# Kernel optimization log

Hardware: AMD Instinct MI355X
Metric: run time of the kernel (lower is better)

Reference implementation:

```python
import jax, jax.numpy as jnp
import numpy as np

HIDDEN = 2048
N_HEADS = 16
HEAD_DIM = HIDDEN // N_HEADS
ROPE_THETA = 10000.0
BSZ, SEQ = 2, 2048
NEG_INF = -1e9


def setup_inputs() -> dict:
    key = jax.random.key(0)
    ks = jax.random.split(key, 5)
    scale = 1.0 / np.sqrt(HIDDEN)
    hidden_states = jax.random.normal(ks[0], (BSZ, SEQ, HIDDEN), dtype=jnp.float32)
    Wq = jax.random.normal(ks[1], (HIDDEN, HIDDEN), dtype=jnp.float32) * scale
    Wk = jax.random.normal(ks[2], (HIDDEN, HIDDEN), dtype=jnp.float32) * scale
    Wv = jax.random.normal(ks[3], (HIDDEN, HIDDEN), dtype=jnp.float32) * scale
    Wo = jax.random.normal(ks[4], (HIDDEN, HIDDEN), dtype=jnp.float32) * scale
    # additive causal mask, [1, 1, S, S]
    causal = jnp.triu(jnp.full((SEQ, SEQ), NEG_INF, dtype=jnp.float32), k=1)
    attention_mask = causal[None, None, :, :]
    position_ids = jnp.arange(SEQ, dtype=jnp.int32)
    return {
        "hidden_states": hidden_states,
        "Wq": Wq, "Wk": Wk, "Wv": Wv, "Wo": Wo,
        "attention_mask": attention_mask,
        "position_ids": position_ids,
    }


def _rotate_half(x):
    half = x.shape[-1] // 2
    return jnp.concatenate((-x[..., half:], x[..., :half]), axis=-1)


def _rope_tables(seq_len, position_ids):
    # inv_freq: [head_dim/2]
    inv_freq = 1.0 / (ROPE_THETA ** (jnp.arange(0, HEAD_DIM, 2, dtype=jnp.float32) / HEAD_DIM))
    t = jnp.arange(seq_len, dtype=jnp.float32)
    freqs = t[:, None] * inv_freq[None, :]              # [S, D/2]
    emb = jnp.concatenate((freqs, freqs), axis=-1)      # [S, D]
    cos = jnp.cos(emb)[position_ids]                    # [S, D]
    sin = jnp.sin(emb)[position_ids]
    return cos, sin


def reference(hidden_states, Wq, Wk, Wv, Wo, attention_mask, position_ids):
    b, s, h = hidden_states.shape
    def proj(W):
        return (hidden_states @ W.T).reshape(b, s, N_HEADS, HEAD_DIM).transpose(0, 2, 1, 3)
    q = proj(Wq)  # [B, H, S, D]
    k = proj(Wk)
    v = proj(Wv)
    cos, sin = _rope_tables(s, position_ids)            # [S, D], broadcasts over B,H
    q = q * cos + _rotate_half(q) * sin
    k = k * cos + _rotate_half(k) * sin
    scores = jnp.einsum('bhqd,bhkd->bhqk', q, k) / np.sqrt(HEAD_DIM)
    scores = scores + attention_mask
    w = jax.nn.softmax(scores, axis=-1)
    out = jnp.einsum('bhqk,bhkd->bhqd', w, v)           # [B, H, S, D]
    out = out.transpose(0, 2, 1, 3).reshape(b, s, h)
    return out @ Wo.T
```

## Files before the change

kernel.cpp:

```cpp
#include <hip/hip_runtime.h>
#include <cstdint>
#include <cstddef>

typedef __bf16 bf16;
typedef __bf16 bf16x4 __attribute__((ext_vector_type(4)));
typedef __bf16 bf16x8 __attribute__((ext_vector_type(8)));
typedef float  f32x4  __attribute__((ext_vector_type(4)));
typedef short  s16x4  __attribute__((ext_vector_type(4)));

#define HIDDEN 2048
#define NHEADS 16
#define HDIM   128
#define BSZ    2
#define SEQ    2048
#define BS     (BSZ*SEQ)
#define QKW    (2*HIDDEN)

union b4u { bf16x4 h; s16x4 s; };

__device__ __forceinline__ void async16(const bf16* g, bf16* l) {
    __builtin_amdgcn_global_load_lds(
        (const __attribute__((address_space(1))) unsigned int*)g,
        (__attribute__((address_space(3))) unsigned int*)l, 16, 0, 0);
}

__global__ __launch_bounds__(256) void cast_all(const float* __restrict__ hs,
                                                const float* __restrict__ Wq,
                                                const float* __restrict__ Wk,
                                                const float* __restrict__ Wv,
                                                const float* __restrict__ Wo,
                                                const int* __restrict__ pos,
                                                bf16* __restrict__ hs_b,
                                                bf16* __restrict__ wqkv,
                                                bf16* __restrict__ wo_b,
                                                float2* __restrict__ tab) {
    int i = blockIdx.x * 256 + threadIdx.x;
    if (i >= 6291456) {
        int j = i - 6291456;
        int s = j >> 6, p = j & 63;
        float t = (float)pos[s];
        float inv = expf(-(float)(2 * p) * (9.2103403719761836f / 128.0f));
        float sn, cs;
        sincosf(t * inv, &sn, &cs);
        tab[j] = make_float2(cs, sn);
        return;
    }
    const float* src; bf16* dst; int off;
    if (i < 2097152) { src = hs; dst = hs_b; off = i; }
    else {
        int j = i - 2097152;
        int r = j >> 20;
        off = j & 1048575;
        if      (r == 0) { src = Wq; dst = wqkv; }
        else if (r == 1) { src = Wk; dst = wqkv + (size_t)4194304; }
        else if (r == 2) { src = Wv; dst = wqkv + (size_t)8388608; }
        else             { src = Wo; dst = wo_b; }
    }
    const float4 v = ((const float4*)src)[off];
    bf16x4 o;
    o.x = (bf16)v.x; o.y = (bf16)v.y; o.z = (bf16)v.z; o.w = (bf16)v.w;
    ((bf16x4*)dst)[off] = o;
}

__global__ __launch_bounds__(256) void gemm_qkv(const bf16* __restrict__ A,
                                                const bf16* __restrict__ Bt,
                                                const float2* __restrict__ tab,
                                                bf16* __restrict__ qk,
                                                bf16* __restrict__ vtb) {
    __shared__ bf16 Als[128 * 32];
    __shared__ bf16 Bls[128 * 32];
    const int K    = HIDDEN;
    const int tid  = threadIdx.x;
    const int lane = tid & 63;
    const int w    = tid >> 6;
    const int l15  = lane & 15;
    const int quad = lane >> 4;
    const int mTile = blockIdx.y * 128;
    const int nTile = blockIdx.x * 128;
    const int wm = (w >> 1) * 64;
    const int wv = w & 1;

    f32x4 acc[4][4];
#pragma unroll
    for (int i = 0; i < 4; ++i)
#pragma unroll
        for (int j = 0; j < 4; ++j) acc[i][j] = (f32x4){0.f, 0.f, 0.f, 0.f};

    const bf16* gA = A + (size_t)(mTile + w * 32 + (lane >> 2)) * K + (lane & 3) * 8;
    const bf16* gB = Bt + (size_t)(nTile + w * 32 + (lane >> 2)) * K + (lane & 3) * 8;
    bf16* lA = Als + w * 1024;
    bf16* lB = Bls + w * 1024;

    for (int k0 = 0; k0 < K; k0 += 32) {
        async16(gA + k0,          lA);
        async16(gA + 16 * K + k0, lA + 512);
        async16(gB + k0,          lB);
        async16(gB + 16 * K + k0, lB + 512);
        __syncthreads();

        bf16x8 af[4], bfr[4];
#pragma unroll
        for (int mi = 0; mi < 4; ++mi)
            af[mi] = *(const bf16x8*)(Als + (wm + mi * 16 + l15) * 32 + quad * 8);
#pragma unroll
        for (int ni = 0; ni < 4; ++ni) {
            int co = wv * 32 + (ni & 1) * 16 + (ni >> 1) * 64;
            bfr[ni] = *(const bf16x8*)(Bls + (co + l15) * 32 + quad * 8);
        }
#pragma unroll
        for (int mi = 0; mi < 4; ++mi)
#pragma unroll
            for (int ni = 0; ni < 4; ++ni)
                acc[mi][ni] = __builtin_amdgcn_mfma_f32_16x16x32_bf16(
                    af[mi], bfr[ni], acc[mi][ni], 0, 0, 0);
        __syncthreads();
    }

    if (nTile < QKW) {
#pragma unroll
        for (int mi = 0; mi < 4; ++mi)
#pragma unroll
            for (int r = 0; r < 4; ++r) {
                int row = mTile + wm + mi * 16 + quad * 4 + r;
                int s   = row & (SEQ - 1);
                float2 t0 = tab[s * 64 + wv * 32 + l15];
                float2 t1 = tab[s * 64 + wv * 32 + 16 + l15];
                size_t rb = (size_t)row * QKW + nTile + wv * 32 + l15;
                float lo0 = acc[mi][0][r], hi0 = acc[mi][2][r];
                float lo1 = acc[mi][1][r], hi1 = acc[mi][3][r];
                qk[rb]      = (bf16)(lo0 * t0.x - hi0 * t0.y);
                qk[rb + 64] = (bf16)(hi0 * t0.x + lo0 * t0.y);
                qk[rb + 16] = (bf16)(lo1 * t1.x - hi1 * t1.y);
                qk[rb + 80] = (bf16)(hi1 * t1.x + lo1 * t1.y);
            }
    } else {
#pragma unroll
        for (int mi = 0; mi < 4; ++mi)
#pragma unroll
            for (int ni = 0; ni < 4; ++ni) {
                int col_v = (nTile - QKW) + wv * 32 + (ni & 1) * 16 + (ni >> 1) * 64 + l15;
                int row0  = mTile + wm + mi * 16 + quad * 4;
                bf16x4 pk;
#pragma unroll
                for (int r = 0; r < 4; ++r) pk[r] = (bf16)acc[mi][ni][r];
                *(bf16x4*)(vtb + (size_t)col_v * BS + row0) = pk;
            }
    }
}

template <typename OutT>
__global__ __launch_bounds__(256) void gemm_bt(const bf16* __restrict__ A,
                                               const bf16* __restrict__ Bt,
                                               OutT* __restrict__ C,
                                               int M, int N, int K) {
    __shared__ bf16 Als[128 * 32];
    __shared__ bf16 Bls[128 * 32];
    const int tid  = threadIdx.x;
    const int lane = tid & 63;
    const int w    = tid >> 6;
    const int l15  = lane & 15;
    const int quad = lane >> 4;
    const int mTile = blockIdx.y * 128;
    const int nTile = blockIdx.x * 128;
    const int wm = (w >> 1) * 64;
    const int wn = (w & 1) * 64;

    f32x4 acc[4][4];
#pragma unroll
    for (int i = 0; i < 4; ++i)
#pragma unroll
        for (int j = 0; j < 4; ++j) acc[i][j] = (f32x4){0.f, 0.f, 0.f, 0.f};

    const bf16* gA = A + (size_t)(mTile + w * 32 + (lane >> 2)) * K + (lane & 3) * 8;
    const bf16* gB = Bt + (size_t)(nTile + w * 32 + (lane >> 2)) * K + (lane & 3) * 8;
    bf16* lA = Als + w * 1024;
    bf16* lB = Bls + w * 1024;

    for (int k0 = 0; k0 < K; k0 += 32) {
        async16(gA + k0,          lA);
        async16(gA + 16 * K + k0, lA + 512);
        async16(gB + k0,          lB);
        async16(gB + 16 * K + k0, lB + 512);
        __syncthreads();

        bf16x8 af[4], bfr[4];
#pragma unroll
        for (int mi = 0; mi < 4; ++mi)
            af[mi] = *(const bf16x8*)(Als + (wm + mi * 16 + l15) * 32 + quad * 8);
#pragma unroll
        for (int ni = 0; ni < 4; ++ni)
            bfr[ni] = *(const bf16x8*)(Bls + (wn + ni * 16 + l15) * 32 + quad * 8);
#pragma unroll
        for (int mi = 0; mi < 4; ++mi)
#pragma unroll
            for (int ni = 0; ni < 4; ++ni)
                acc[mi][ni] = __builtin_amdgcn_mfma_f32_16x16x32_bf16(
                    af[mi], bfr[ni], acc[mi][ni], 0, 0, 0);
        __syncthreads();
    }

#pragma unroll
    for (int mi = 0; mi < 4; ++mi)
#pragma unroll
        for (int ni = 0; ni < 4; ++ni)
#pragma unroll
            for (int r = 0; r < 4; ++r) {
                int row = mTile + wm + mi * 16 + quad * 4 + r;
                int col = nTile + wn + ni * 16 + l15;
                C[(size_t)row * N + col] = (OutT)acc[mi][ni][r];
            }
}

__global__ __launch_bounds__(256) void attn_kernel(const bf16* __restrict__ qk,
                                                   const bf16* __restrict__ vt,
                                                   bf16* __restrict__ ao) {
    __shared__ bf16 Kls[64 * 128];
    __shared__ bf16 Vls[128 * 64];

    const int tid  = threadIdx.x;
    const int lane = tid & 63;
    const int w    = tid >> 6;
    const int l15  = lane & 15;
    const int quad = lane >> 4;
    const int bid  = blockIdx.x;
    const int qt   = 31 - (bid >> 5);
    const int bh   = bid & 31;
    const int b    = bh >> 4;
    const int h    = bh & 15;
    const int qbase = qt * 64;
    const size_t seq0 = (size_t)b * SEQ;

    bf16x8 qf[4];
    {
        const bf16* qp = qk + (seq0 + qbase + w * 16 + l15) * QKW + h * HDIM + quad * 8;
#pragma unroll
        for (int ks = 0; ks < 4; ++ks) qf[ks] = *(const bf16x8*)(qp + ks * 32);
    }

    f32x4 o[8];
#pragma unroll
    for (int i = 0; i < 8; ++i) o[i] = (f32x4){0.f, 0.f, 0.f, 0.f};
    float m_s = -3e38f, l_s = 0.f;
    const int qg = qbase + w * 16 + l15;

    const int krow = lane >> 4;
    const int kp   = lane & 15;
    const int vrow = lane >> 3;
    const int vp   = lane & 7;
    const int sw   = l15 & 7;

    for (int t = 0; t <= qt; ++t) {
        const int kb = t * 64;
#pragma unroll
        for (int i = 0; i < 4; ++i) {
            int j = w * 16 + i * 4 + krow;
            int c = (kp & 8) | ((kp & 7) ^ (j & 7));
            async16(qk + (seq0 + kb + j) * QKW + HIDDEN + h * HDIM + c * 8,
                    Kls + (w * 4 + i) * 512);
        }
#pragma unroll
        for (int i = 0; i < 4; ++i) {
            int d = w * 32 + i * 8 + vrow;
            int c = vp ^ (d & 7);
            async16(vt + (size_t)(h * HDIM + d) * (size_t)BS + seq0 + kb + c * 8,
                    Vls + (w * 4 + i) * 512);
        }
        __syncthreads();

        f32x4 sa[4];
#pragma unroll
        for (int ni = 0; ni < 4; ++ni) sa[ni] = (f32x4){0.f, 0.f, 0.f, 0.f};
#pragma unroll
        for (int ni = 0; ni < 4; ++ni)
#pragma unroll
            for (int ks = 0; ks < 4; ++ks) {
                bf16x8 kf = *(const bf16x8*)(Kls + (ni * 16 + l15) * 128 +
                                             (((ks * 4 + quad) ^ sw) << 3));
                sa[ni] = __builtin_amdgcn_mfma_f32_16x16x32_bf16(kf, qf[ks], sa[ni], 0, 0, 0);
            }

        const float scale = 0.08838834764831845f * 1.4426950408889634f;
        float rmax = -3e38f;
        const bool diag = (t == qt);
#pragma unroll
        for (int ni = 0; ni < 4; ++ni)
#pragma unroll
            for (int r = 0; r < 4; ++r) {
                float sv = sa[ni][r] * scale;
                if (diag) {
                    int jg = kb + ni * 16 + quad * 4 + r;
                    if (jg > qg) sv = -1e30f;
                }
                sa[ni][r] = sv;
                rmax = fmaxf(rmax, sv);
            }
        rmax = fmaxf(rmax, __shfl_xor(rmax, 16));
        rmax = fmaxf(rmax, __shfl_xor(rmax, 32));

        float mn = fmaxf(m_s, rmax);
        float alpha = exp2f(m_s - mn);
        m_s = mn;
        float rsum = 0.f;
        b4u pb[4];
#pragma unroll
        for (int ni = 0; ni < 4; ++ni)
#pragma unroll
            for (int r = 0; r < 4; ++r) {
                float e = exp2f(sa[ni][r] - mn);
                rsum += e;
                pb[ni].h[r] = (bf16)e;
            }
        rsum += __shfl_xor(rsum, 16);
        rsum += __shfl_xor(rsum, 32);
        l_s = l_s * alpha + rsum;

        if (__ballot(alpha != 1.f) != 0ull) {
#pragma unroll
            for (int n2 = 0; n2 < 8; ++n2)
#pragma unroll
                for (int r = 0; r < 4; ++r) o[n2][r] *= alpha;
        }

#pragma unroll
        for (int n2 = 0; n2 < 8; ++n2)
#pragma unroll
            for (int ni = 0; ni < 4; ++ni) {
                b4u vf;
                vf.h = *(const bf16x4*)(Vls + (n2 * 16 + l15) * 64 +
                                        ((((ni * 2 + (quad >> 1)) ^ sw) << 3) + (quad & 1) * 4));
                o[n2] = __builtin_amdgcn_mfma_f32_16x16x16bf16_1k(vf.s, pb[ni].s, o[n2], 0, 0, 0);
            }
        __syncthreads();
    }

    const float inv = 1.0f / l_s;
    bf16* op = ao + (seq0 + qg) * HIDDEN + h * HDIM + quad * 4;
#pragma unroll
    for (int n2 = 0; n2 < 8; ++n2) {
        bf16x4 pk;
#pragma unroll
        for (int r = 0; r < 4; ++r) pk[r] = (bf16)(o[n2][r] * inv);
        *(bf16x4*)(op + n2 * 16) = pk;
    }
}

extern "C" void kernel_launch(void* const* d_in, const int* in_sizes, int n_in,
                              void* d_out, int out_size, void* d_ws, size_t ws_size,
                              hipStream_t stream) {
    const float* hs = (const float*)d_in[0];
    const float* Wq = (const float*)d_in[1];
    const float* Wk = (const float*)d_in[2];
    const float* Wv = (const float*)d_in[3];
    const float* Wo = (const float*)d_in[4];
    const int* pos  = (const int*)d_in[6];
    float* out = (float*)d_out;

    bf16* hs_b = (bf16*)d_ws;
    bf16* wqkv = hs_b + (size_t)8388608;
    bf16* wo_b = wqkv + (size_t)12582912;
    bf16* qkb  = wo_b + (size_t)4194304;
    bf16* vtb  = qkb + (size_t)16777216;
    bf16* ao   = vtb + (size_t)8388608;
    float2* tab = (float2*)ao;

    cast_all<<<25088, 256, 0, stream>>>(hs, Wq, Wk, Wv, Wo, pos, hs_b, wqkv, wo_b, tab);
    gemm_qkv<<<dim3(48, 32), 256, 0, stream>>>(hs_b, wqkv, tab, qkb, vtb);
    attn_kernel<<<1024, 256, 0, stream>>>(qkb, vtb, ao);
    gemm_bt<float><<<dim3(HIDDEN / 128, BS / 128), 256, 0, stream>>>(ao, wo_b, out, BS, HIDDEN, HIDDEN);
}
```

Before: 397.6 us.

## Rewrite QKV GEMM with 256x256 tiles and a 4-stage async LDS pipeline

The QKV projection GEMM moves from 128x128 tiles with 4 waves and a single LDS buffer to 256x256 tiles with 8 waves, a 4-deep ring of LDS buffers filled by async global-to-LDS loads, XOR-swizzled LDS columns, and raw s_barrier/vmcnt waits around split MFMA phases with setprio. Block IDs are remapped so neighbouring workgroups share tiles in L2, and B rows for Q/K are permuted so the RoPE epilogue still pairs lo/hi halves. The goal is to hide global load latency and raise arithmetic intensity per LDS byte. In exchange it uses 128KB of LDS and many more accumulator registers, and the hand-written wait counts and buffer indexing must be exactly right to stay correct.

```diff
diff --git a/kernel.cpp b/kernel.cpp
--- a/kernel.cpp
+++ b/kernel.cpp
@@ -23,6 +23,9 @@
         (const __attribute__((address_space(1))) unsigned int*)g,
         (__attribute__((address_space(3))) unsigned int*)l, 16, 0, 0);
 }
+
+#define BARX()  asm volatile("s_barrier" ::: "memory")
+#define VMW(N)  asm volatile("s_waitcnt vmcnt(" #N ")" ::: "memory")
 
 __global__ __launch_bounds__(256) void cast_all(const float* __restrict__ hs,
                                                 const float* __restrict__ Wq,
@@ -62,72 +65,119 @@
     ((bf16x4*)dst)[off] = o;
 }
 
-__global__ __launch_bounds__(256) void gemm_qkv(const bf16* __restrict__ A,
-                                                const bf16* __restrict__ Bt,
-                                                const float2* __restrict__ tab,
-                                                bf16* __restrict__ qk,
-                                                bf16* __restrict__ vtb) {
-    __shared__ bf16 Als[128 * 32];
-    __shared__ bf16 Bls[128 * 32];
-    const int K    = HIDDEN;
+__device__ __forceinline__ int qk_perm(int n) {
+    int wl = n >> 6, j = n & 63;
+    return ((wl >> 1) << 7) | ((j >> 5) << 6) | ((wl & 1) << 5) | (j & 31);
+}
+
+#define QKV_TILE(T, DOSTAGE, VMN) do {                                          \
+    const int bufR_ = (T) & 3;                                                  \
+    const bf16* lAr = smem + bufR_ * 16384 + (wm * 128 + l15) * 32 + colE;      \
+    const bf16* lBr = smem + bufR_ * 16384 + 8192 + (wn * 64 + l15) * 32 + colE;\
+    bf16x8 bfr[4], af[4];                                                       \
+    _Pragma("unroll") for (int nf = 0; nf < 4; ++nf)                            \
+        bfr[nf] = *(const bf16x8*)(lBr + nf * 512);                             \
+    _Pragma("unroll") for (int mf = 0; mf < 4; ++mf)                            \
+        af[mf] = *(const bf16x8*)(lAr + mf * 512);                              \
+    if (DOSTAGE) {                                                              \
+        bf16* dA = smem + (((T) + 3) & 3) * 16384 + w * 512;                    \
+        async16(pa0 + ((T) + 3) * 32, dA);                                      \
+        async16(pa1 + ((T) + 3) * 32, dA + 4096);                               \
+    }                                                                           \
+    BARX();                                                                     \
+    __builtin_amdgcn_s_setprio(1);                                              \
+    _Pragma("unroll") for (int mf = 0; mf < 4; ++mf)                            \
+    _Pragma("unroll") for (int nf = 0; nf < 4; ++nf)                            \
+        acc[mf][nf] = __builtin_amdgcn_mfma_f32_16x16x32_bf16(                  \
+            af[mf], bfr[nf], acc[mf][nf], 0, 0, 0);                             \
+    __builtin_amdgcn_s_setprio(0);                                              \
+    BARX();                                                                     \
+    _Pragma("unroll") for (int mf = 0; mf < 4; ++mf)                            \
+        af[mf] = *(const bf16x8*)(lAr + 2048 + mf * 512);                       \
+    if (DOSTAGE) {                                                              \
+        bf16* dB = smem + (((T) + 3) & 3) * 16384 + 8192 + w * 512;             \
+        async16(pb0 + ((T) + 3) * 32, dB);                                      \
+        async16(pb1 + ((T) + 3) * 32, dB + 4096);                               \
+    }                                                                           \
+    VMW(VMN);                                                                   \
+    BARX();                                                                     \
+    __builtin_amdgcn_s_setprio(1);                                              \
+    _Pragma("unroll") for (int mf = 0; mf < 4; ++mf)                            \
+    _Pragma("unroll") for (int nf = 0; nf < 4; ++nf)                            \
+        acc[4 + mf][nf] = __builtin_amdgcn_mfma_f32_16x16x32_bf16(              \
+            af[mf], bfr[nf], acc[4 + mf][nf], 0, 0, 0);                         \
+    __builtin_amdgcn_s_setprio(0);                                              \
+    BARX();                                                                     \
+} while (0)
+
+__global__ __launch_bounds__(512, 2) void gemm_qkv(const bf16* __restrict__ A,
+                                                   const bf16* __restrict__ Bt,
+                                                   const float2* __restrict__ tab,
+                                                   bf16* __restrict__ qk,
+                                                   bf16* __restrict__ vtb) {
+    __shared__ alignas(16) bf16 smem[65536];
+
     const int tid  = threadIdx.x;
     const int lane = tid & 63;
     const int w    = tid >> 6;
     const int l15  = lane & 15;
     const int quad = lane >> 4;
-    const int mTile = blockIdx.y * 128;
-    const int nTile = blockIdx.x * 128;
-    const int wm = (w >> 1) * 64;
-    const int wv = w & 1;
-
-    f32x4 acc[4][4];
-#pragma unroll
-    for (int i = 0; i < 4; ++i)
+    const int wm   = w >> 2;
+    const int wn   = w & 3;
+
+    int raw = blockIdx.y * 24 + blockIdx.x;
+    int wg  = (raw & 7) * 48 + (raw >> 3);
+    const int mTile = (wg / 24) * 256;
+    const int nTile = (wg % 24) * 256;
+
+    const int sRow  = w * 16 + (lane >> 2);
+    const int sColE = ((lane & 3) * 8) ^ ((lane & 32) ? 16 : 0);
+    const bf16* pa0 = A + (size_t)(mTile + sRow) * HIDDEN + sColE;
+    const bf16* pa1 = pa0 + (size_t)128 * HIDDEN;
+    int n0 = sRow, n1 = sRow + 128;
+    if (nTile < QKW) { n0 = qk_perm(n0); n1 = qk_perm(n1); }
+    const bf16* pb0 = Bt + (size_t)(nTile + n0) * HIDDEN + sColE;
+    const bf16* pb1 = Bt + (size_t)(nTile + n1) * HIDDEN + sColE;
+
+    const int colE = (quad * 8) ^ ((l15 & 8) ? 16 : 0);
+
+    f32x4 acc[8][4];
+#pragma unroll
+    for (int i = 0; i < 8; ++i)
 #pragma unroll
         for (int j = 0; j < 4; ++j) acc[i][j] = (f32x4){0.f, 0.f, 0.f, 0.f};
 
-    const bf16* gA = A + (size_t)(mTile + w * 32 + (lane >> 2)) * K + (lane & 3) * 8;
-    const bf16* gB = Bt + (size_t)(nTile + w * 32 + (lane >> 2)) * K + (lane & 3) * 8;
-    bf16* lA = Als + w * 1024;
-    bf16* lB = Bls + w * 1024;
-
-    for (int k0 = 0; k0 < K; k0 += 32) {
-        async16(gA + k0,          lA);
-        async16(gA + 16 * K + k0, lA + 512);
-        async16(gB + k0,          lB);
-        async16(gB + 16 * K + k0, lB + 512);
-        __syncthreads();
-
-        bf16x8 af[4], bfr[4];
-#pragma unroll
-        for (int mi = 0; mi < 4; ++mi)
-            af[mi] = *(const bf16x8*)(Als + (wm + mi * 16 + l15) * 32 + quad * 8);
-#pragma unroll
-        for (int ni = 0; ni < 4; ++ni) {
-            int co = wv * 32 + (ni & 1) * 16 + (ni >> 1) * 64;
-            bfr[ni] = *(const bf16x8*)(Bls + (co + l15) * 32 + quad * 8);
-        }
-#pragma unroll
-        for (int mi = 0; mi < 4; ++mi)
-#pragma unroll
-            for (int ni = 0; ni < 4; ++ni)
-                acc[mi][ni] = __builtin_amdgcn_mfma_f32_16x16x32_bf16(
-                    af[mi], bfr[ni], acc[mi][ni], 0, 0, 0);
-        __syncthreads();
-    }
+#pragma unroll
+    for (int tt = 0; tt < 3; ++tt) {
+        bf16* dA = smem + tt * 16384 + w * 512;
+        async16(pa0 + tt * 32, dA);
+        async16(pa1 + tt * 32, dA + 4096);
+        async16(pb0 + tt * 32, dA + 8192);
+        async16(pb1 + tt * 32, dA + 8192 + 4096);
+    }
+    VMW(8);
+    BARX();
+
+#pragma unroll 4
+    for (int t = 0; t < 60; ++t) QKV_TILE(t, 1, 8);
+    QKV_TILE(60, 1, 8);
+    QKV_TILE(61, 0, 4);
+    QKV_TILE(62, 0, 0);
+    QKV_TILE(63, 0, 0);
 
     if (nTile < QKW) {
-#pragma unroll
-        for (int mi = 0; mi < 4; ++mi)
+        const int hbase = nTile + (wn >> 1) * 128 + (wn & 1) * 32;
+#pragma unroll
+        for (int mf = 0; mf < 8; ++mf)
 #pragma unroll
             for (int r = 0; r < 4; ++r) {
-                int row = mTile + wm + mi * 16 + quad * 4 + r;
+                int row = mTile + wm * 128 + mf * 16 + quad * 4 + r;
                 int s   = row & (SEQ - 1);
-                float2 t0 = tab[s * 64 + wv * 32 + l15];
-                float2 t1 = tab[s * 64 + wv * 32 + 16 + l15];
-                size_t rb = (size_t)row * QKW + nTile + wv * 32 + l15;
-                float lo0 = acc[mi][0][r], hi0 = acc[mi][2][r];
-                float lo1 = acc[mi][1][r], hi1 = acc[mi][3][r];
+                float2 t0 = tab[s * 64 + (wn & 1) * 32 + l15];
+                float2 t1 = tab[s * 64 + (wn & 1) * 32 + 16 + l15];
+                size_t rb = (size_t)row * QKW + hbase + l15;
+                float lo0 = acc[mf][0][r], hi0 = acc[mf][2][r];
+                float lo1 = acc[mf][1][r], hi1 = acc[mf][3][r];
                 qk[rb]      = (bf16)(lo0 * t0.x - hi0 * t0.y);
                 qk[rb + 64] = (bf16)(hi0 * t0.x + lo0 * t0.y);
                 qk[rb + 16] = (bf16)(lo1 * t1.x - hi1 * t1.y);
@@ -135,14 +185,14 @@
             }
     } else {
 #pragma unroll
-        for (int mi = 0; mi < 4; ++mi)
-#pragma unroll
-            for (int ni = 0; ni < 4; ++ni) {
-                int col_v = (nTile - QKW) + wv * 32 + (ni & 1) * 16 + (ni >> 1) * 64 + l15;
-                int row0  = mTile + wm + mi * 16 + quad * 4;
+        for (int mf = 0; mf < 8; ++mf)
+#pragma unroll
+            for (int nf = 0; nf < 4; ++nf) {
+                int col_v = (nTile - QKW) + wn * 64 + nf * 16 + l15;
+                int row0  = mTile + wm * 128 + mf * 16 + quad * 4;
                 bf16x4 pk;
 #pragma unroll
-                for (int r = 0; r < 4; ++r) pk[r] = (bf16)acc[mi][ni][r];
+                for (int r = 0; r < 4; ++r) pk[r] = (bf16)acc[mf][nf][r];
                 *(bf16x4*)(vtb + (size_t)col_v * BS + row0) = pk;
             }
     }
@@ -364,7 +414,7 @@
     float2* tab = (float2*)ao;
 
     cast_all<<<25088, 256, 0, stream>>>(hs, Wq, Wk, Wv, Wo, pos, hs_b, wqkv, wo_b, tab);
-    gemm_qkv<<<dim3(48, 32), 256, 0, stream>>>(hs_b, wqkv, tab, qkb, vtb);
+    gemm_qkv<<<dim3(24, 16), 512, 0, stream>>>(hs_b, wqkv, tab, qkb, vtb);
     attn_kernel<<<1024, 256, 0, stream>>>(qkb, vtb, ao);
     gemm_bt<float><<<dim3(HIDDEN / 128, BS / 128), 256, 0, stream>>>(ao, wo_b, out, BS, HIDDEN, HIDDEN);
 }
```

New measurement: 408.4 us. 1.03x slower.
